# Performance work log

Measured on AMD Instinct MI355X. Metric: run time of the kernel, lower is better.

The kernel has to match this reference:

```python
import jax, jax.numpy as jnp
import numpy as np

N = 1_000_000      # neurons
E = 16_000_000     # connections (edges)
NIN = 1024         # input vector length
NOUT = 8192        # output neurons gathered
REFRACTORY = 0.33  # config['refractory_factor']
CLIP = 1.0         # config['relu_clip_at']
NUM_ACTS = 8       # identity, relu, leaky_relu, clipped_relu, tanh, sigmoid, softplus, abs


def setup_inputs() -> dict:
    key = jax.random.key(0)
    ks = jax.random.split(key, 10)
    state = jax.random.normal(ks[0], (N,), dtype=jnp.float32)
    weights = jax.random.normal(ks[1], (E,), dtype=jnp.float32) * 0.1
    biases = jax.random.normal(ks[2], (N,), dtype=jnp.float32) * 0.1
    inp = jax.random.normal(ks[3], (NIN,), dtype=jnp.float32)
    src = jax.random.randint(ks[4], (E,), 0, N, dtype=jnp.int32)
    dst = jax.random.randint(ks[5], (E,), 0, N, dtype=jnp.int32)
    rec_mask = jax.random.randint(ks[6], (E,), 0, 2, dtype=jnp.int32).astype(bool)
    input_idx = jax.random.randint(ks[7], (E,), 0, NIN, dtype=jnp.int32)
    act_id = jax.random.randint(ks[8], (N,), 0, NUM_ACTS, dtype=jnp.int32)
    out_ids = jax.random.randint(ks[9], (NOUT,), 0, N, dtype=jnp.int32)
    return {"state": state, "weights": weights, "biases": biases, "inp": inp,
            "src": src, "dst": dst, "rec_mask": rec_mask,
            "input_idx": input_idx, "act_id": act_id, "out_ids": out_ids}


def _apply_activations(x, act_id):
    # Per-neuron activation select; ids follow ActivationFunctions order.
    acts = jnp.stack([
        x,                                   # identity
        jax.nn.relu(x),                      # relu
        jax.nn.leaky_relu(x),                # leaky_relu (default slope 0.01)
        jnp.clip(x, 0.0, CLIP),              # clipped_relu
        jnp.tanh(x),                         # tanh
        jax.nn.sigmoid(x),                   # sigmoid
        jax.nn.softplus(x),                  # softplus
        jnp.abs(x),                          # abs
    ])  # [8, N]
    return acts[act_id, jnp.arange(x.shape[0])]


def reference(state, weights, biases, inp, src, dst, rec_mask, input_idx, act_id, out_ids):
    # Shallow dict copy + in-place *= in torch scales the accumulation base too.
    prev = REFRACTORY * state                                    # [N]
    # Per-edge source value: recurrent edges read prev state, others read input.
    from_state = jnp.where(rec_mask, prev[src], inp[input_idx])  # [E]
    msg = weights * from_state                                   # [E]
    acc = prev + jax.ops.segment_sum(msg, dst, num_segments=N) + biases  # [N]
    new_state = _apply_activations(acc, act_id)                  # [N]
    return new_state[out_ids]                                    # [NOUT]
```

## Files before the change

kernel.cpp:

```cpp
#include <hip/hip_runtime.h>
#include <math.h>

#define REFRACTORY 0.33f
#define FILT_WORDS 32768
#define QCAP 2048

#define WS_ACC_OFF 256

__global__ void setup(const unsigned int* __restrict__ rm, int nwords,
                      int* __restrict__ flag,
                      const int* __restrict__ out_ids,
                      const float* __restrict__ state,
                      const float* __restrict__ biases,
                      float* __restrict__ acc, int nout) {
    if (blockIdx.x == 0) {
        __shared__ int s;
        if (threadIdx.x == 0) s = 0;
        __syncthreads();
        int found = 0;
        for (int i = threadIdx.x; i < nwords; i += blockDim.x)
            if (rm[i] > 1u) found = 1;
        if (found) atomicOr(&s, 1);
        __syncthreads();
        if (threadIdx.x == 0) *flag = s;
    } else {
        int i = (blockIdx.x - 1) * blockDim.x + threadIdx.x;
        if (i < nout) {
            int n = out_ids[i];
            acc[n] = REFRACTORY * state[n] + biases[n];
        }
    }
}

__device__ __forceinline__ void process_edge(
    int d, int e,
    const float* __restrict__ w, const int* __restrict__ src,
    const unsigned char* __restrict__ rmb, const int* __restrict__ input_idx,
    const float* __restrict__ state, const float* __restrict__ inp,
    float* __restrict__ acc, int bytemode) {
    int m = bytemode ? (int)rmb[e] : ((const int*)rmb)[e];
    float v = m ? REFRACTORY * state[src[e]] : inp[input_idx[e]];
    unsafeAtomicAdd(&acc[d], w[e] * v);
}

__global__ void __launch_bounds__(1024, 1)
edge_fused(const int* __restrict__ dst,
           const int* __restrict__ out_ids, int nout,
           int E, int shift,
           const float* __restrict__ w, const int* __restrict__ src,
           const unsigned char* __restrict__ rmb,
           const int* __restrict__ input_idx,
           const float* __restrict__ state, const float* __restrict__ inp,
           float* __restrict__ acc,
           const int* __restrict__ flag) {
    __shared__ unsigned int filt[FILT_WORDS];
    __shared__ int2 lq[QCAP];
    __shared__ int lcnt;

    {
        uint4* f4 = (uint4*)filt;
        uint4 z = make_uint4(0, 0, 0, 0);
        for (int i = threadIdx.x; i < FILT_WORDS / 4; i += blockDim.x)
            f4[i] = z;
    }
    if (threadIdx.x == 0) lcnt = 0;
    __syncthreads();
    for (int i = threadIdx.x; i < nout; i += blockDim.x) {
        unsigned g = ((unsigned)out_ids[i]) >> shift;
        atomicOr(&filt[g >> 5], 1u << (g & 31));
    }
    __syncthreads();

    const int bytemode = *flag;
    const int sh5 = shift + 5;
    int gtid = blockIdx.x * blockDim.x + threadIdx.x;
    int gstride = gridDim.x * blockDim.x;
    int nq = E >> 2;
    const int4* d4p = (const int4*)dst;

#define SLOT(dv, ev, valid)                                                    \
    {                                                                          \
        unsigned dd = (unsigned)(dv);                                          \
        bool c = (valid) && ((filt[dd >> sh5] >> ((dd >> shift) & 31)) & 1u);  \
        if (c) {                                                               \
            int off = atomicAdd(&lcnt, 1);                                     \
            if (off < QCAP) lq[off] = make_int2((ev), (int)dd);                \
            else process_edge((int)dd, (ev), w, src, rmb, input_idx,           \
                              state, inp, acc, bytemode);                      \
        }                                                                      \
    }

    for (int t = gtid; t < nq; t += 2 * gstride) {
        int4 A = d4p[t];
        int t2 = t + gstride;
        bool has2 = (t2 < nq);
        int4 B = has2 ? d4p[t2] : make_int4(0, 0, 0, 0);
        int ea = t << 2;
        SLOT(A.x, ea + 0, true);
        SLOT(A.y, ea + 1, true);
        SLOT(A.z, ea + 2, true);
        SLOT(A.w, ea + 3, true);
        int eb = t2 << 2;
        SLOT(B.x, eb + 0, has2);
        SLOT(B.y, eb + 1, has2);
        SLOT(B.z, eb + 2, has2);
        SLOT(B.w, eb + 3, has2);
    }
#undef SLOT

    int rem = E - nq * 4;
    if (gtid < rem) {
        int e = nq * 4 + gtid;
        int d = dst[e];
        process_edge(d, e, w, src, rmb, input_idx, state, inp, acc, bytemode);
    }

    __syncthreads();
    int n = lcnt < QCAP ? lcnt : QCAP;
    for (int i = threadIdx.x; i < n; i += blockDim.x) {
        int2 c = lq[i];
        process_edge(c.y, c.x, w, src, rmb, input_idx, state, inp, acc, bytemode);
    }
}

__global__ void gather_out(const float* __restrict__ acc,
                           const int* __restrict__ act_id,
                           const int* __restrict__ out_ids,
                           float* __restrict__ out, int nout) {
    int i = blockIdx.x * blockDim.x + threadIdx.x;
    if (i >= nout) return;
    int n = out_ids[i];
    float x = acc[n];
    float y;
    switch (act_id[n]) {
        case 0: y = x; break;
        case 1: y = fmaxf(x, 0.0f); break;
        case 2: y = x > 0.0f ? x : 0.01f * x; break;
        case 3: y = fminf(fmaxf(x, 0.0f), 1.0f); break;
        case 4: y = tanhf(x); break;
        case 5: y = 1.0f / (1.0f + expf(-x)); break;
        case 6: y = fmaxf(x, 0.0f) + log1pf(expf(-fabsf(x))); break;
        default: y = fabsf(x); break;
    }
    out[i] = y;
}

extern "C" void kernel_launch(void* const* d_in, const int* in_sizes, int n_in,
                              void* d_out, int out_size, void* d_ws, size_t ws_size,
                              hipStream_t stream) {
    const float* state     = (const float*)d_in[0];
    const float* weights   = (const float*)d_in[1];
    const float* biases    = (const float*)d_in[2];
    const float* inp       = (const float*)d_in[3];
    const int*   src       = (const int*)d_in[4];
    const int*   dst       = (const int*)d_in[5];
    const void*  rec_mask  = d_in[6];
    const int*   input_idx = (const int*)d_in[7];
    const int*   act_id    = (const int*)d_in[8];
    const int*   out_ids   = (const int*)d_in[9];
    float*       out       = (float*)d_out;

    const int N = in_sizes[0];
    const int E = in_sizes[1];
    const int NOUT = out_size;

    int*   flag = (int*)d_ws;
    float* acc  = (float*)((char*)d_ws + WS_ACC_OFF);

    int shift = 0;
    while ((((long long)N + ((1LL << shift) - 1)) >> shift) > (long long)FILT_WORDS * 32)
        shift++;

    int nwords = E / 4;
    if (nwords > 2048) nwords = 2048;
    if (nwords < 1) nwords = 1;
    int setupBlocks = 1 + (NOUT + 255) / 256;
    setup<<<setupBlocks, 256, 0, stream>>>((const unsigned int*)rec_mask, nwords,
                                           flag, out_ids, state, biases, acc, NOUT);

    edge_fused<<<256, 1024, 0, stream>>>(
        dst, out_ids, NOUT, E, shift,
        weights, src, (const unsigned char*)rec_mask, input_idx,
        state, inp, acc, flag);

    gather_out<<<(NOUT + 255) / 256, 256, 0, stream>>>(acc, act_id, out_ids, out, NOUT);
}
```

Before: 42.36 us.

## Shrink LDS filter for higher occupancy and add exact global bitmap check

New measurement: 50.88 us. +20.1%, slower.

```diff
diff --git a/kernel.cpp b/kernel.cpp
--- a/kernel.cpp
+++ b/kernel.cpp
@@ -2,17 +2,18 @@
 #include <math.h>
 
 #define REFRACTORY 0.33f
-#define FILT_WORDS 32768
-#define QCAP 2048
-
-#define WS_ACC_OFF 256
+#define FILT_WORDS 8192
+#define QCAP 768
+
+#define WS_BM_OFF  256
+#define WS_ACC_OFF (256 + 131072)
 
 __global__ void setup(const unsigned int* __restrict__ rm, int nwords,
                       int* __restrict__ flag,
-                      const int* __restrict__ out_ids,
-                      const float* __restrict__ state,
-                      const float* __restrict__ biases,
-                      float* __restrict__ acc, int nout) {
+                      unsigned int* __restrict__ bm, int bmWords) {
+    int gid = blockIdx.x * blockDim.x + threadIdx.x;
+    int stride = gridDim.x * blockDim.x;
+    for (int i = gid; i < bmWords; i += stride) bm[i] = 0u;
     if (blockIdx.x == 0) {
         __shared__ int s;
         if (threadIdx.x == 0) s = 0;
@@ -23,13 +24,19 @@
         if (found) atomicOr(&s, 1);
         __syncthreads();
         if (threadIdx.x == 0) *flag = s;
-    } else {
-        int i = (blockIdx.x - 1) * blockDim.x + threadIdx.x;
-        if (i < nout) {
-            int n = out_ids[i];
-            acc[n] = REFRACTORY * state[n] + biases[n];
-        }
-    }
+    }
+}
+
+__global__ void mark_init(const int* __restrict__ out_ids,
+                          const float* __restrict__ state,
+                          const float* __restrict__ biases,
+                          unsigned int* __restrict__ bm,
+                          float* __restrict__ acc, int nout) {
+    int i = blockIdx.x * blockDim.x + threadIdx.x;
+    if (i >= nout) return;
+    int n = out_ids[i];
+    atomicOr(&bm[((unsigned)n) >> 5], 1u << (n & 31));
+    acc[n] = REFRACTORY * state[n] + biases[n];
 }
 
 __device__ __forceinline__ void process_edge(
@@ -43,10 +50,11 @@
     unsafeAtomicAdd(&acc[d], w[e] * v);
 }
 
-__global__ void __launch_bounds__(1024, 1)
+__global__ void __launch_bounds__(256, 4)
 edge_fused(const int* __restrict__ dst,
            const int* __restrict__ out_ids, int nout,
            int E, int shift,
+           const unsigned int* __restrict__ bm,
            const float* __restrict__ w, const int* __restrict__ src,
            const unsigned char* __restrict__ rmb,
            const int* __restrict__ input_idx,
@@ -85,8 +93,9 @@
         if (c) {                                                               \
             int off = atomicAdd(&lcnt, 1);                                     \
             if (off < QCAP) lq[off] = make_int2((ev), (int)dd);                \
-            else process_edge((int)dd, (ev), w, src, rmb, input_idx,           \
-                              state, inp, acc, bytemode);                      \
+            else if ((bm[dd >> 5] >> (dd & 31)) & 1u)                          \
+                process_edge((int)dd, (ev), w, src, rmb, input_idx,            \
+                             state, inp, acc, bytemode);                       \
         }                                                                      \
     }
 
@@ -119,7 +128,9 @@
     int n = lcnt < QCAP ? lcnt : QCAP;
     for (int i = threadIdx.x; i < n; i += blockDim.x) {
         int2 c = lq[i];
-        process_edge(c.y, c.x, w, src, rmb, input_idx, state, inp, acc, bytemode);
+        unsigned d = (unsigned)c.y;
+        if ((bm[d >> 5] >> (d & 31)) & 1u)
+            process_edge(c.y, c.x, w, src, rmb, input_idx, state, inp, acc, bytemode);
     }
 }
 
@@ -164,8 +175,11 @@
     const int E = in_sizes[1];
     const int NOUT = out_size;
 
-    int*   flag = (int*)d_ws;
-    float* acc  = (float*)((char*)d_ws + WS_ACC_OFF);
+    int*          flag = (int*)d_ws;
+    unsigned int* bm   = (unsigned int*)((char*)d_ws + WS_BM_OFF);
+    float*        acc  = (float*)((char*)d_ws + WS_ACC_OFF);
+
+    const int bmWords = (N + 31) / 32;
 
     int shift = 0;
     while ((((long long)N + ((1LL << shift) - 1)) >> shift) > (long long)FILT_WORDS * 32)
@@ -174,12 +188,14 @@
     int nwords = E / 4;
     if (nwords > 2048) nwords = 2048;
     if (nwords < 1) nwords = 1;
-    int setupBlocks = 1 + (NOUT + 255) / 256;
-    setup<<<setupBlocks, 256, 0, stream>>>((const unsigned int*)rec_mask, nwords,
-                                           flag, out_ids, state, biases, acc, NOUT);
-
-    edge_fused<<<256, 1024, 0, stream>>>(
-        dst, out_ids, NOUT, E, shift,
+    setup<<<64, 256, 0, stream>>>((const unsigned int*)rec_mask, nwords,
+                                  flag, bm, bmWords);
+
+    mark_init<<<(NOUT + 255) / 256, 256, 0, stream>>>(out_ids, state, biases,
+                                                      bm, acc, NOUT);
+
+    edge_fused<<<1024, 256, 0, stream>>>(
+        dst, out_ids, NOUT, E, shift, bm,
         weights, src, (const unsigned char*)rec_mask, input_idx,
         state, inp, acc, flag);
 
```

## Build output-neuron bitmap once globally and copy into shared filter; unroll dst loop 4x

Applied to the files above, without the earlier changes.

After: 47.51 us. 12.1% more time.

```diff
diff --git a/kernel.cpp b/kernel.cpp
--- a/kernel.cpp
+++ b/kernel.cpp
@@ -5,14 +5,16 @@
 #define FILT_WORDS 32768
 #define QCAP 2048
 
-#define WS_ACC_OFF 256
+#define WS_BM_OFF  256
+#define WS_ACC_OFF (256 + 131072)
 
-__global__ void setup(const unsigned int* __restrict__ rm, int nwords,
-                      int* __restrict__ flag,
-                      const int* __restrict__ out_ids,
-                      const float* __restrict__ state,
-                      const float* __restrict__ biases,
-                      float* __restrict__ acc, int nout) {
+__global__ void mark_init(const unsigned int* __restrict__ rm, int nwords,
+                          int* __restrict__ flag,
+                          const int* __restrict__ out_ids,
+                          const float* __restrict__ state,
+                          const float* __restrict__ biases,
+                          unsigned int* __restrict__ bm,
+                          float* __restrict__ acc, int nout) {
     if (blockIdx.x == 0) {
         __shared__ int s;
         if (threadIdx.x == 0) s = 0;
@@ -27,6 +29,7 @@
         int i = (blockIdx.x - 1) * blockDim.x + threadIdx.x;
         if (i < nout) {
             int n = out_ids[i];
+            atomicOr(&bm[((unsigned)n) >> 5], 1u << (n & 31));
             acc[n] = REFRACTORY * state[n] + biases[n];
         }
     }
@@ -45,8 +48,8 @@
 
 __global__ void __launch_bounds__(1024, 1)
 edge_fused(const int* __restrict__ dst,
-           const int* __restrict__ out_ids, int nout,
-           int E, int shift,
+           const unsigned int* __restrict__ bm,
+           int E,
            const float* __restrict__ w, const int* __restrict__ src,
            const unsigned char* __restrict__ rmb,
            const int* __restrict__ input_idx,
@@ -58,21 +61,15 @@
     __shared__ int lcnt;
 
     {
+        const uint4* g4 = (const uint4*)bm;
         uint4* f4 = (uint4*)filt;
-        uint4 z = make_uint4(0, 0, 0, 0);
         for (int i = threadIdx.x; i < FILT_WORDS / 4; i += blockDim.x)
-            f4[i] = z;
+            f4[i] = g4[i];
     }
     if (threadIdx.x == 0) lcnt = 0;
     __syncthreads();
-    for (int i = threadIdx.x; i < nout; i += blockDim.x) {
-        unsigned g = ((unsigned)out_ids[i]) >> shift;
-        atomicOr(&filt[g >> 5], 1u << (g & 31));
-    }
-    __syncthreads();
 
     const int bytemode = *flag;
-    const int sh5 = shift + 5;
     int gtid = blockIdx.x * blockDim.x + threadIdx.x;
     int gstride = gridDim.x * blockDim.x;
     int nq = E >> 2;
@@ -81,7 +78,7 @@
 #define SLOT(dv, ev, valid)                                                    \
     {                                                                          \
         unsigned dd = (unsigned)(dv);                                          \
-        bool c = (valid) && ((filt[dd >> sh5] >> ((dd >> shift) & 31)) & 1u);  \
+        bool c = (valid) && ((filt[dd >> 5] >> (dd & 31)) & 1u);               \
         if (c) {                                                               \
             int off = atomicAdd(&lcnt, 1);                                     \
             if (off < QCAP) lq[off] = make_int2((ev), (int)dd);                \
@@ -90,21 +87,33 @@
         }                                                                      \
     }
 
-    for (int t = gtid; t < nq; t += 2 * gstride) {
+    for (int t = gtid; t < nq; t += 4 * gstride) {
+        int tB = t + gstride, tC = t + 2 * gstride, tD = t + 3 * gstride;
+        bool hB = tB < nq, hC = tC < nq, hD = tD < nq;
         int4 A = d4p[t];
-        int t2 = t + gstride;
-        bool has2 = (t2 < nq);
-        int4 B = has2 ? d4p[t2] : make_int4(0, 0, 0, 0);
+        int4 B = hB ? d4p[tB] : make_int4(0, 0, 0, 0);
+        int4 C = hC ? d4p[tC] : make_int4(0, 0, 0, 0);
+        int4 D = hD ? d4p[tD] : make_int4(0, 0, 0, 0);
         int ea = t << 2;
         SLOT(A.x, ea + 0, true);
         SLOT(A.y, ea + 1, true);
         SLOT(A.z, ea + 2, true);
         SLOT(A.w, ea + 3, true);
-        int eb = t2 << 2;
-        SLOT(B.x, eb + 0, has2);
-        SLOT(B.y, eb + 1, has2);
-        SLOT(B.z, eb + 2, has2);
-        SLOT(B.w, eb + 3, has2);
+        int eb = tB << 2;
+        SLOT(B.x, eb + 0, hB);
+        SLOT(B.y, eb + 1, hB);
+        SLOT(B.z, eb + 2, hB);
+        SLOT(B.w, eb + 3, hB);
+        int ec = tC << 2;
+        SLOT(C.x, ec + 0, hC);
+        SLOT(C.y, ec + 1, hC);
+        SLOT(C.z, ec + 2, hC);
+        SLOT(C.w, ec + 3, hC);
+        int ed = tD << 2;
+        SLOT(D.x, ed + 0, hD);
+        SLOT(D.y, ed + 1, hD);
+        SLOT(D.z, ed + 2, hD);
+        SLOT(D.w, ed + 3, hD);
     }
 #undef SLOT
 
@@ -160,26 +169,25 @@
     const int*   out_ids   = (const int*)d_in[9];
     float*       out       = (float*)d_out;
 
-    const int N = in_sizes[0];
     const int E = in_sizes[1];
     const int NOUT = out_size;
 
-    int*   flag = (int*)d_ws;
-    float* acc  = (float*)((char*)d_ws + WS_ACC_OFF);
+    int*          flag = (int*)d_ws;
+    unsigned int* bm   = (unsigned int*)((char*)d_ws + WS_BM_OFF);
+    float*        acc  = (float*)((char*)d_ws + WS_ACC_OFF);
 
-    int shift = 0;
-    while ((((long long)N + ((1LL << shift) - 1)) >> shift) > (long long)FILT_WORDS * 32)
-        shift++;
+    hipMemsetAsync(bm, 0, FILT_WORDS * 4, stream);
 
     int nwords = E / 4;
     if (nwords > 2048) nwords = 2048;
     if (nwords < 1) nwords = 1;
-    int setupBlocks = 1 + (NOUT + 255) / 256;
-    setup<<<setupBlocks, 256, 0, stream>>>((const unsigned int*)rec_mask, nwords,
-                                           flag, out_ids, state, biases, acc, NOUT);
+    int markBlocks = 1 + (NOUT + 255) / 256;
+    mark_init<<<markBlocks, 256, 0, stream>>>((const unsigned int*)rec_mask, nwords,
+                                              flag, out_ids, state, biases,
+                                              bm, acc, NOUT);
 
     edge_fused<<<256, 1024, 0, stream>>>(
-        dst, out_ids, NOUT, E, shift,
+        dst, bm, E,
         weights, src, (const unsigned char*)rec_mask, input_idx,
         state, inp, acc, flag);
 
```

## Use per-wave LDS queues with threshold draining instead of one block queue

Applied to the files above, without the earlier changes.

Result: faster. 37.79 us, median of 3 (-10.8%).

```diff
diff --git a/kernel.cpp b/kernel.cpp
--- a/kernel.cpp
+++ b/kernel.cpp
@@ -3,7 +3,9 @@
 
 #define REFRACTORY 0.33f
 #define FILT_WORDS 32768
-#define QCAP 2048
+#define QWCAP 128
+#define NWAVES 16
+#define DRAIN_THRESH 16
 
 #define WS_ACC_OFF 256
 
@@ -54,8 +56,8 @@
            float* __restrict__ acc,
            const int* __restrict__ flag) {
     __shared__ unsigned int filt[FILT_WORDS];
-    __shared__ int2 lq[QCAP];
-    __shared__ int lcnt;
+    __shared__ int2 lq[NWAVES * QWCAP];
+    __shared__ int wcnt[NWAVES];
 
     {
         uint4* f4 = (uint4*)filt;
@@ -63,7 +65,7 @@
         for (int i = threadIdx.x; i < FILT_WORDS / 4; i += blockDim.x)
             f4[i] = z;
     }
-    if (threadIdx.x == 0) lcnt = 0;
+    if ((threadIdx.x & 63) == 0) wcnt[threadIdx.x >> 6] = 0;
     __syncthreads();
     for (int i = threadIdx.x; i < nout; i += blockDim.x) {
         unsigned g = ((unsigned)out_ids[i]) >> shift;
@@ -72,41 +74,62 @@
     __syncthreads();
 
     const int bytemode = *flag;
-    const int sh5 = shift + 5;
+    const int lane = threadIdx.x & 63;
+    const int wv = threadIdx.x >> 6;
+    int2* wq = &lq[wv * QWCAP];
+    int* mycnt = &wcnt[wv];
+
     int gtid = blockIdx.x * blockDim.x + threadIdx.x;
     int gstride = gridDim.x * blockDim.x;
     int nq = E >> 2;
     const int4* d4p = (const int4*)dst;
 
-#define SLOT(dv, ev, valid)                                                    \
-    {                                                                          \
-        unsigned dd = (unsigned)(dv);                                          \
-        bool c = (valid) && ((filt[dd >> sh5] >> ((dd >> shift) & 31)) & 1u);  \
-        if (c) {                                                               \
-            int off = atomicAdd(&lcnt, 1);                                     \
-            if (off < QCAP) lq[off] = make_int2((ev), (int)dd);                \
-            else process_edge((int)dd, (ev), w, src, rmb, input_idx,           \
-                              state, inp, acc, bytemode);                      \
-        }                                                                      \
-    }
+#define PROBE(dv, hv, k)                                                       \
+    { unsigned dd = (unsigned)(dv) >> shift;                                   \
+      hv |= ((filt[dd >> 5] >> (dd & 31)) & 1u) << (k); }
+
+#define ENQ(ev, dv)                                                            \
+    { int off = atomicAdd(mycnt, 1);                                           \
+      if (off < QWCAP) wq[off] = make_int2((ev), (int)(dv));                   \
+      else process_edge((int)(dv), (ev), w, src, rmb, input_idx,               \
+                        state, inp, acc, bytemode); }
 
     for (int t = gtid; t < nq; t += 2 * gstride) {
+        int tB = t + gstride;
+        bool vB = tB < nq;
         int4 A = d4p[t];
-        int t2 = t + gstride;
-        bool has2 = (t2 < nq);
-        int4 B = has2 ? d4p[t2] : make_int4(0, 0, 0, 0);
-        int ea = t << 2;
-        SLOT(A.x, ea + 0, true);
-        SLOT(A.y, ea + 1, true);
-        SLOT(A.z, ea + 2, true);
-        SLOT(A.w, ea + 3, true);
-        int eb = t2 << 2;
-        SLOT(B.x, eb + 0, has2);
-        SLOT(B.y, eb + 1, has2);
-        SLOT(B.z, eb + 2, has2);
-        SLOT(B.w, eb + 3, has2);
-    }
-#undef SLOT
+        int4 B = vB ? d4p[tB] : make_int4(0, 0, 0, 0);
+
+        unsigned mA = 0, mB = 0;
+        PROBE(A.x, mA, 0) PROBE(A.y, mA, 1) PROBE(A.z, mA, 2) PROBE(A.w, mA, 3)
+        PROBE(B.x, mB, 0) PROBE(B.y, mB, 1) PROBE(B.z, mB, 2) PROBE(B.w, mB, 3)
+        if (!vB) mB = 0;
+
+        if (mA | mB) {
+            int ea = t << 2, eb = tB << 2;
+            if (mA & 1) ENQ(ea + 0, A.x)
+            if (mA & 2) ENQ(ea + 1, A.y)
+            if (mA & 4) ENQ(ea + 2, A.z)
+            if (mA & 8) ENQ(ea + 3, A.w)
+            if (mB & 1) ENQ(eb + 0, B.x)
+            if (mB & 2) ENQ(eb + 1, B.y)
+            if (mB & 4) ENQ(eb + 2, B.z)
+            if (mB & 8) ENQ(eb + 3, B.w)
+        }
+
+        int have = *mycnt;
+        if (have >= DRAIN_THRESH) {
+            int nn = have < QWCAP ? have : QWCAP;
+            for (int i = lane; i < nn; i += 64) {
+                int2 c = wq[i];
+                process_edge(c.y, c.x, w, src, rmb, input_idx,
+                             state, inp, acc, bytemode);
+            }
+            if (lane == 0) *mycnt = 0;
+        }
+    }
+#undef PROBE
+#undef ENQ
 
     int rem = E - nq * 4;
     if (gtid < rem) {
@@ -115,11 +138,14 @@
         process_edge(d, e, w, src, rmb, input_idx, state, inp, acc, bytemode);
     }
 
-    __syncthreads();
-    int n = lcnt < QCAP ? lcnt : QCAP;
-    for (int i = threadIdx.x; i < n; i += blockDim.x) {
-        int2 c = lq[i];
-        process_edge(c.y, c.x, w, src, rmb, input_idx, state, inp, acc, bytemode);
+    {
+        int have = *mycnt;
+        int nn = have < QWCAP ? have : QWCAP;
+        for (int i = lane; i < nn; i += 64) {
+            int2 c = wq[i];
+            process_edge(c.y, c.x, w, src, rmb, input_idx,
+                         state, inp, acc, bytemode);
+        }
     }
 }
 
```
